# Performance work log

Hardware: AMD Instinct MI355X
Metric: run time of the kernel (lower is better)

Reference implementation:

```python
import jax, jax.numpy as jnp
import numpy as np
from jax.scipy.linalg import solve_triangular

H = 4          # num_heads
CHUNK = 64     # delta-rule chunk size (math-equivalent to any chunking)
NORM_EPS = 1e-5


def setup_inputs() -> dict:
    key = jax.random.key(0)
    ks = jax.random.split(key, 9)
    B, L, D = 4, 4096, 1024
    dk, dv = 512, 1024
    s = 0.02  # ~ xavier_uniform gain 2**-2.5 scale
    return {
        "hidden_states": jax.random.normal(ks[0], (B, L, D), jnp.float32),
        "conv_w": jax.random.normal(ks[1], (D, 4), jnp.float32) * 0.2,
        "Wq": jax.random.normal(ks[2], (D, dk), jnp.float32) * s,
        "Wk": jax.random.normal(ks[3], (D, dk), jnp.float32) * s,
        "Wv": jax.random.normal(ks[4], (D, dv), jnp.float32) * s,
        "Wb": jax.random.normal(ks[5], (D, H), jnp.float32) * s,
        "Wg": jax.random.normal(ks[6], (D, dv), jnp.float32) * s,
        "norm_w": jnp.ones((dv // H,), jnp.float32),
        "Wo": jax.random.normal(ks[7], (dv, D), jnp.float32) * s,
    }


def _l2norm(x):
    return x / jnp.clip(jnp.linalg.norm(x, axis=-1, keepdims=True), 1e-12)


def _deltanet_forward(hidden_states, conv_w, Wq, Wk, Wv, Wb, Wg, norm_w, Wo):
    B, L, D = hidden_states.shape
    Kc = conv_w.shape[1]
    dqh = Wq.shape[1] // H   # head qk dim (128)
    dvh = Wv.shape[1] // H   # head v dim (256)

    # shared causal depthwise short conv + silu (ShortConvolution)
    xp = jnp.pad(hidden_states, ((0, 0), (Kc - 1, 0), (0, 0)))
    h = sum(conv_w[:, i] * xp[:, i:i + L, :] for i in range(Kc))
    h = jax.nn.silu(h)

    q = (h @ Wq).reshape(B, L, H, dqh).transpose(0, 2, 1, 3)  # b h l d
    k = (h @ Wk).reshape(B, L, H, dqh).transpose(0, 2, 1, 3)
    v = (h @ Wv).reshape(B, L, H, dvh).transpose(0, 2, 1, 3)
    q = _l2norm(q)
    k = _l2norm(k)
    beta = jax.nn.sigmoid(h @ Wb).transpose(0, 2, 1)          # b h l

    qm = q.reshape(B * H, L, dqh)
    km = k.reshape(B * H, L, dqh)
    vm = v.reshape(B * H, L, dvh)
    bm = beta.reshape(B * H, L)

    Nc = L // CHUNK
    eye = jnp.eye(CHUNK, dtype=q.dtype)

    def per_head(qh, kh, vh, bh):
        qs = qh.reshape(Nc, CHUNK, dqh)
        ks_ = kh.reshape(Nc, CHUNK, dqh)
        vs = vh.reshape(Nc, CHUNK, dvh)
        bs = bh.reshape(Nc, CHUNK)

        def step(S, xs):
            qc, kc, vc, bc = xs
            kb = kc * bc[:, None]
            # (I + strict_tril(kb k^T)) U = beta*(V - K S)  -> exact delta rule
            A = jnp.tril(kb @ kc.T, -1)
            U = solve_triangular(eye + A, vc * bc[:, None] - kb @ S, lower=True)
            o = qc @ S + jnp.tril(qc @ kc.T) @ U
            return S + kc.T @ U, o

        S0 = jnp.zeros((dqh, dvh), qh.dtype)
        _, o = jax.lax.scan(step, S0, (qs, ks_, vs, bs))
        return o.reshape(L, dvh)

    o = jax.vmap(per_head)(qm, km, vm, bm)                    # (B*H, L, dvh)
    o = o.reshape(B, H, L, dvh).transpose(0, 2, 1, 3)         # b l h d

    # FusedRMSNormSwishGate: rmsnorm(o) * weight * silu(g)
    g = (h @ Wg).reshape(B, L, H, dvh)
    rms = o * jax.lax.rsqrt(jnp.mean(o * o, axis=-1, keepdims=True) + NORM_EPS)
    out = rms * norm_w * (g * jax.nn.sigmoid(g))
    return out.reshape(B, L, H * dvh) @ Wo


def reference(hidden_states, conv_w, Wq, Wk, Wv, Wb, Wg, norm_w, Wo):
    return _deltanet_forward(hidden_states, conv_w, Wq, Wk, Wv, Wb, Wg, norm_w, Wo)
```

## Files before the change

### kernel.cpp

```cpp
#include <hip/hip_runtime.h>
#include <math.h>

constexpr int Lseq = 4096, Dm = 1024, H = 4, DK = 512, DV = 1024;
constexpr int DQH = 128, DVH = 256, CH = 64, ROWS = 4 * 4096;
constexpr int QKS = 1024;

typedef unsigned short u16;
struct alignas(16) us8 { u16 u[8]; };
typedef __attribute__((ext_vector_type(8))) short bf16x8;
typedef __attribute__((ext_vector_type(4))) float f32x4;

__device__ __forceinline__ float sig_(float x) { return 1.f / (1.f + expf(-x)); }
__device__ __forceinline__ float b2f(u16 u) {
  union { float f; unsigned v; } x; x.v = (unsigned)u << 16; return x.f;
}
__device__ __forceinline__ u16 f2b(float f) {
  union { float f; unsigned v; } x; x.f = f;
  unsigned r = x.v + 0x7fffu + ((x.v >> 16) & 1u);
  return (u16)(r >> 16);
}
__device__ __forceinline__ void gld16(const u16* g, u16* l) {
  __builtin_amdgcn_global_load_lds(
      (const __attribute__((address_space(1))) void*)g,
      (__attribute__((address_space(3))) void*)l, 16, 0, 0);
}

__global__ void ws_sentinel_kernel(float* out, float v) { out[0] = v; }

__global__ __launch_bounds__(256) void prologue_kernel(
    const float* __restrict__ x, const float* __restrict__ w, u16* __restrict__ h,
    const float* __restrict__ Wq, const float* __restrict__ Wk,
    const float* __restrict__ Wv, const float* __restrict__ Wg,
    const float* __restrict__ Wo,
    u16* wq16, u16* wk16, u16* wv16, u16* wg16, u16* wo16) {
  __shared__ u16 T[32][66];
  const int t = threadIdx.x;
  if (blockIdx.x < 8192) {
    int idx = blockIdx.x * 256 + t;
    int d8 = (idx & 127) << 3;
    int row = idx >> 7;
    int l = row & (Lseq - 1), b = row >> 12;
    const float* xb = x + ((size_t)b << 22);
    float4 wv_[8];
#pragma unroll
    for (int j = 0; j < 2; ++j) {
      wv_[j * 4 + 0] = *(const float4*)&w[d8 * 4 + j * 16 + 0];
      wv_[j * 4 + 1] = *(const float4*)&w[d8 * 4 + j * 16 + 4];
      wv_[j * 4 + 2] = *(const float4*)&w[d8 * 4 + j * 16 + 8];
      wv_[j * 4 + 3] = *(const float4*)&w[d8 * 4 + j * 16 + 12];
    }
    float acc[8] = {0, 0, 0, 0, 0, 0, 0, 0};
#pragma unroll
    for (int i = 0; i < 4; ++i) {
      int li = l - 3 + i;
      if (li >= 0) {
        float4 x0 = *(const float4*)&xb[((size_t)li << 10) + d8];
        float4 x1 = *(const float4*)&xb[((size_t)li << 10) + d8 + 4];
        acc[0] = fmaf(((const float*)&wv_[0])[i], x0.x, acc[0]);
        acc[1] = fmaf(((const float*)&wv_[1])[i], x0.y, acc[1]);
        acc[2] = fmaf(((const float*)&wv_[2])[i], x0.z, acc[2]);
        acc[3] = fmaf(((const float*)&wv_[3])[i], x0.w, acc[3]);
        acc[4] = fmaf(((const float*)&wv_[4])[i], x1.x, acc[4]);
        acc[5] = fmaf(((const float*)&wv_[5])[i], x1.y, acc[5]);
        acc[6] = fmaf(((const float*)&wv_[6])[i], x1.z, acc[6]);
        acc[7] = fmaf(((const float*)&wv_[7])[i], x1.w, acc[7]);
      }
    }
    us8 o;
#pragma unroll
    for (int j = 0; j < 8; ++j) o.u[j] = f2b(acc[j] * sig_(acc[j]));
    *(us8*)&h[(size_t)row * Dm + d8] = o;
    return;
  }
  int bid = blockIdx.x - 8192;
  const float* in; u16* out; int N, K, b0;
  if (bid < 256)       { in = Wq; out = wq16; N = DK; K = Dm; b0 = bid; }
  else if (bid < 512)  { in = Wk; out = wk16; N = DK; K = Dm; b0 = bid - 256; }
  else if (bid < 1024) { in = Wv; out = wv16; N = DV; K = Dm; b0 = bid - 512; }
  else if (bid < 1536) { in = Wg; out = wg16; N = DV; K = Dm; b0 = bid - 1024; }
  else                 { in = Wo; out = wo16; N = Dm; K = DV; b0 = bid - 1536; }
  const int nbx = N / 64;
  const int k0 = (b0 / nbx) * 32, n0 = (b0 % nbx) * 64;
#pragma unroll
  for (int i = 0; i < 8; ++i) {
    int idx = t + i * 256;
    int kk = idx >> 6, nn = idx & 63;
    T[kk][nn] = f2b(in[(size_t)(k0 + kk) * N + n0 + nn]);
  }
  __syncthreads();
#pragma unroll
  for (int i = 0; i < 8; ++i) {
    int idx = t + i * 256;
    int kk = idx & 31, nn = idx >> 5;
    out[(size_t)(n0 + nn) * K + k0 + kk] = T[kk][nn];
  }
}

template <int MODE>
__device__ __forceinline__ void gemm_body(
    const u16* __restrict__ A, const u16* __restrict__ BT, void* __restrict__ Cv,
    int M, int N, int K, int bid, int nwg, u16* As, u16* Bs) {
  const int tid = threadIdx.x;
  const int wid = tid >> 6, lane = tid & 63;
  const int wr = wid >> 1, wc = wid & 1;
  const int fr = lane & 15, fk = lane >> 4;
  const int nbx = N >> 7;
  const int swz = (bid & 7) * (nwg >> 3) + (bid >> 3);
  const int row0 = (swz / nbx) * 128, col0 = (swz % nbx) * 128;

  int sr[4], sk[4];
#pragma unroll
  for (int i = 0; i < 4; ++i) {
    int s = i * 4 + wid;
    int r = s * 8 + (lane >> 3);
    sr[i] = r;
    sk[i] = ((lane & 7) ^ (r & 7)) << 3;
  }

  f32x4 acc[4][4];
#pragma unroll
  for (int i = 0; i < 4; ++i)
#pragma unroll
    for (int j = 0; j < 4; ++j) acc[i][j] = {0.f, 0.f, 0.f, 0.f};

  for (int k0 = 0; k0 < K; k0 += 64) {
#pragma unroll
    for (int i = 0; i < 4; ++i) {
      const int s = i * 4 + wid;
      gld16(&A[(size_t)(row0 + sr[i]) * K + k0 + sk[i]], &As[s * 512]);
      gld16(&BT[(size_t)(col0 + sr[i]) * K + k0 + sk[i]], &Bs[s * 512]);
    }
    __syncthreads();
#pragma unroll
    for (int kt = 0; kt < 2; ++kt) {
      bf16x8 af[4], bf[4];
#pragma unroll
      for (int mi = 0; mi < 4; ++mi) {
        int row = wr * 64 + mi * 16 + fr;
        af[mi] = *(const bf16x8*)&As[row * 64 + (((kt * 4 + fk) ^ (fr & 7)) << 3)];
      }
#pragma unroll
      for (int ni = 0; ni < 4; ++ni) {
        int row = wc * 64 + ni * 16 + fr;
        bf[ni] = *(const bf16x8*)&Bs[row * 64 + (((kt * 4 + fk) ^ (fr & 7)) << 3)];
      }
#pragma unroll
      for (int mi = 0; mi < 4; ++mi)
#pragma unroll
        for (int ni = 0; ni < 4; ++ni)
          acc[mi][ni] = __builtin_amdgcn_mfma_f32_16x16x32_bf16(
              af[mi], bf[ni], acc[mi][ni], 0, 0, 0);
    }
    __syncthreads();
  }

  if (MODE == 2) {
    __shared__ float ssh[2][128];
#pragma unroll
    for (int mi = 0; mi < 4; ++mi)
#pragma unroll
      for (int r = 0; r < 4; ++r) {
        float p = 0.f;
#pragma unroll
        for (int ni = 0; ni < 4; ++ni) p += acc[mi][ni][r] * acc[mi][ni][r];
        p += __shfl_xor(p, 1); p += __shfl_xor(p, 2);
        p += __shfl_xor(p, 4); p += __shfl_xor(p, 8);
        if (fr == 0) ssh[wc][wr * 64 + mi * 16 + fk * 4 + r] = p;
      }
    __syncthreads();
#pragma unroll
    for (int mi = 0; mi < 4; ++mi)
#pragma unroll
      for (int r = 0; r < 4; ++r) {
        int ridx = wr * 64 + mi * 16 + fk * 4 + r;
        float sc = 1.f / fmaxf(sqrtf(ssh[0][ridx] + ssh[1][ridx]), 1e-12f);
#pragma unroll
        for (int ni = 0; ni < 4; ++ni) acc[mi][ni][r] *= sc;
      }
  }

#pragma unroll
  for (int mi = 0; mi < 4; ++mi)
#pragma unroll
    for (int ni = 0; ni < 4; ++ni) {
      int col = col0 + wc * 64 + ni * 16 + fr;
#pragma unroll
      for (int r = 0; r < 4; ++r) {
        int row = row0 + wr * 64 + mi * 16 + fk * 4 + r;
        if (MODE == 1) ((float*)Cv)[(size_t)row * N + col] = acc[mi][ni][r];
        else           ((u16*)Cv)[(size_t)row * N + col] = f2b(acc[mi][ni][r]);
      }
    }
}

__global__ __launch_bounds__(256) void gemm_mfma_kernel(
    const u16* __restrict__ A, const u16* __restrict__ BT, void* __restrict__ Cv,
    int M, int N, int K) {
  __shared__ u16 As[128 * 64];
  __shared__ u16 Bs[128 * 64];
  gemm_body<1>(A, BT, Cv, M, N, K, blockIdx.x, gridDim.x, As, Bs);
}

__global__ __launch_bounds__(256) void proj_kernel(
    const u16* __restrict__ hb, const u16* __restrict__ wqk16,
    const u16* __restrict__ wv16, const float* __restrict__ Wb,
    u16* __restrict__ qk, u16* __restrict__ vb, float* __restrict__ beta) {
  __shared__ u16 As[128 * 64];
  __shared__ u16 Bs[128 * 64];
  const int bid = blockIdx.x;
  if (bid < 1024) {
    gemm_body<2>(hb, wqk16, qk, ROWS, QKS, Dm, bid, 1024, As, Bs);
    return;
  }
  if (bid < 2048) {
    gemm_body<0>(hb, wv16, vb, ROWS, DV, Dm, bid - 1024, 1024, As, Bs);
    return;
  }
  int row = (bid - 2048) * 4 + (threadIdx.x >> 6), lane = threadIdx.x & 63;
  const u16* hrow = hb + (size_t)row * Dm;
  float a0 = 0, a1 = 0, a2 = 0, a3 = 0;
  for (int k0 = 0; k0 < Dm; k0 += 64) {
    float hv = b2f(hrow[k0 + lane]);
    float4 wv = *(const float4*)&Wb[(size_t)(k0 + lane) * 4];
    a0 = fmaf(hv, wv.x, a0); a1 = fmaf(hv, wv.y, a1);
    a2 = fmaf(hv, wv.z, a2); a3 = fmaf(hv, wv.w, a3);
  }
#pragma unroll
  for (int off = 32; off; off >>= 1) {
    a0 += __shfl_down(a0, off); a1 += __shfl_down(a1, off);
    a2 += __shfl_down(a2, off); a3 += __shfl_down(a3, off);
  }
  if (lane == 0) {
    int b = row >> 12, l = row & (Lseq - 1);
    beta[((size_t)(b * H + 0)) * Lseq + l] = sig_(a0);
    beta[((size_t)(b * H + 1)) * Lseq + l] = sig_(a1);
    beta[((size_t)(b * H + 2)) * Lseq + l] = sig_(a2);
    beta[((size_t)(b * H + 3)) * Lseq + l] = sig_(a3);
  }
}

__global__ __launch_bounds__(256) void delta_prep_kernel(
    const u16* __restrict__ qk, u16* v, const float* __restrict__ beta,
    u16* __restrict__ Wout, u16* __restrict__ QKout) {
  __shared__ alignas(16) char lds0[18432];
  __shared__ alignas(16) char lds1[18432];
  __shared__ float Bc[64];
  float (*Am)[68] = (float(*)[68])lds0;
  float (*R)[68]  = (float(*)[68])lds1;
  u16 (*Th)[72]  = (u16(*)[72])lds0;
  u16 (*Tl)[72]  = (u16(*)[72])(lds0 + 9216);
  u16 (*XTh)[72] = (u16(*)[72])lds1;
  u16 (*XTl)[72] = (u16(*)[72])(lds1 + 9216);

  const int tid = threadIdx.x;
  const int wid = tid >> 6, lane = tid & 63;
  const int fr = lane & 15, fq = lane >> 4;
  const int bh = blockIdx.x >> 6, ch = blockIdx.x & 63;
  const int b = bh >> 2, hh = bh & 3;
  const int c0 = ch * CH;
  const u16* qbase = qk + (size_t)b * Lseq * QKS + hh * DQH;
  const u16* kbase = qk + (size_t)b * Lseq * QKS + 512 + hh * DQH;
  u16*       vbase = v + (size_t)b * Lseq * DV + hh * DVH;
  const float* bbase = beta + (size_t)bh * Lseq;
  u16* Wrow  = Wout  + ((size_t)bh * Lseq + c0) * DQH;
  u16* QKrow = QKout + ((size_t)bh * Lseq + c0) * CH;

  if (tid < 64) Bc[tid] = bbase[c0 + tid];
  for (int idx = tid; idx < 64 * 64; idx += 256) {
    int r = idx >> 6, c = idx & 63;
    R[r][c] = (r == c) ? 1.f : 0.f;
  }
  __syncthreads();

  {
    const int m0 = wid * 16;
    f32x4 accG[4], accQ[4];
#pragma unroll
    for (int ni = 0; ni < 4; ++ni) {
      accG[ni] = {0.f, 0.f, 0.f, 0.f};
      accQ[ni] = {0.f, 0.f, 0.f, 0.f};
    }
#pragma unroll
    for (int kt = 0; kt < 4; ++kt) {
      bf16x8 afk = *(const bf16x8*)&kbase[(size_t)(c0 + m0 + fr) * QKS + kt * 32 + fq * 8];
      bf16x8 afq = *(const bf16x8*)&qbase[(size_t)(c0 + m0 + fr) * QKS + kt * 32 + fq * 8];
#pragma unroll
      for (int ni = 0; ni < 4; ++ni) {
        bf16x8 bfk = *(const bf16x8*)&kbase[(size_t)(c0 + ni * 16 + fr) * QKS + kt * 32 + fq * 8];
        accG[ni] = __builtin_amdgcn_mfma_f32_16x16x32_bf16(afk, bfk, accG[ni], 0, 0, 0);
        accQ[ni] = __builtin_amdgcn_mfma_f32_16x16x32_bf16(afq, bfk, accQ[ni], 0, 0, 0);
      }
    }
#pragma unroll
    for (int ni = 0; ni < 4; ++ni)
#pragma unroll
      for (int i = 0; i < 4; ++i) {
        int row = m0 + fq * 4 + i, col = ni * 16 + fr;
        float br = Bc[row];
        Am[row][col] = (col < row) ? br * accG[ni][i] : 0.f;
        QKrow[(size_t)row * CH + col] = f2b((col <= row) ? accQ[ni][i] : 0.f);
      }
  }
  __syncthreads();

  for (int rb = 0; rb < 4; ++rb) {
    if (rb > 0) {
      const int c = tid & 63, g = tid >> 6;
      const int R0 = rb * 16, row = R0 + g * 4;
      float s0 = 0, s1 = 0, s2 = 0, s3 = 0;
      for (int m = 0; m < R0; ++m) {
        float uv = R[m][c];
        s0 = fmaf(Am[row + 0][m], uv, s0);
        s1 = fmaf(Am[row + 1][m], uv, s1);
        s2 = fmaf(Am[row + 2][m], uv, s2);
        s3 = fmaf(Am[row + 3][m], uv, s3);
      }
      R[row + 0][c] -= s0; R[row + 1][c] -= s1;
      R[row + 2][c] -= s2; R[row + 3][c] -= s3;
    }
    __syncthreads();
    if (tid < 64) {
      const int c = tid;
      for (int i = 1; i < 16; ++i) {
        const int row = rb * 16 + i;
        float s = R[row][c];
        for (int m = 0; m < i; ++m)
          s = fmaf(-Am[row][rb * 16 + m], R[rb * 16 + m][c], s);
        R[row][c] = s;
      }
    }
    __syncthreads();
  }

  for (int idx = tid; idx < 64 * 64; idx += 256) {
    int r = idx >> 6, c = idx & 63;
    float tv = R[r][c];
    u16 hh2 = f2b(tv);
    Th[r][c] = hh2;
    Tl[r][c] = f2b(tv - b2f(hh2));
  }
  __syncthreads();

  for (int p = 0; p < 6; ++p) {
    const int off = (p < 2) ? p * 64 : (p - 2) * 64;
    for (int idx = tid; idx < 64 * 64; idx += 256) {
      int d = idx & 63, m = idx >> 6;
      float xv;
      if (p < 2) xv = Bc[m] * b2f(kbase[(size_t)(c0 + m) * QKS + off + d]);
      else       xv = Bc[m] * b2f(vbase[(size_t)(c0 + m) * DV + off + d]);
      u16 hh2 = f2b(xv);
      XTh[d][m] = hh2;
      XTl[d][m] = f2b(xv - b2f(hh2));
    }
    __syncthreads();
    f32x4 acc[4];
#pragma unroll
    for (int tn = 0; tn < 4; ++tn) acc[tn] = {0.f, 0.f, 0.f, 0.f};
#pragma unroll
    for (int kt = 0; kt < 2; ++kt) {
      bf16x8 ah = *(const bf16x8*)&Th[wid * 16 + fr][kt * 32 + fq * 8];
      bf16x8 al = *(const bf16x8*)&Tl[wid * 16 + fr][kt * 32 + fq * 8];
#pragma unroll
      for (int tn = 0; tn < 4; ++tn) {
        bf16x8 xh = *(const bf16x8*)&XTh[tn * 16 + fr][kt * 32 + fq * 8];
        bf16x8 xl = *(const bf16x8*)&XTl[tn * 16 + fr][kt * 32 + fq * 8];
        acc[tn] = __builtin_amdgcn_mfma_f32_16x16x32_bf16(ah, xh, acc[tn], 0, 0, 0);
        acc[tn] = __builtin_amdgcn_mfma_f32_16x16x32_bf16(ah, xl, acc[tn], 0, 0, 0);
        acc[tn] = __builtin_amdgcn_mfma_f32_16x16x32_bf16(al, xh, acc[tn], 0, 0, 0);
      }
    }
#pragma unroll
    for (int tn = 0; tn < 4; ++tn)
#pragma unroll
      for (int i = 0; i < 4; ++i) {
        int row = wid * 16 + fq * 4 + i, col = tn * 16 + fr;
        if (p < 2) Wrow[(size_t)row * DQH + off + col] = f2b(-acc[tn][i]);
        else       vbase[(size_t)(c0 + row) * DV + off + col] = f2b(acc[tn][i]);
      }
    __syncthreads();
  }
}

__device__ __forceinline__ void scan_body(
    int sbid, const u16* __restrict__ qkp,
    const u16* __restrict__ Wb, const u16* __restrict__ QKb, u16* uo,
    u16 (*Kt)[72], u16 (*Sbt_hi)[136], u16 (*Sbt_lo)[136], u16 (*Ubt)[72]) {
  const int tid = threadIdx.x;
  const int wid = tid >> 6, lane = tid & 63;
  const int fr = lane & 15, fq = lane >> 4;
  const int m0w = 16 * (wid & 3);
  const int bh = sbid & 15, vblk = sbid >> 4;
  const int b = bh >> 2, hh = bh & 3;
  const u16* qbase = qkp + (size_t)b * Lseq * QKS + hh * DQH;
  const u16* kbase = qkp + (size_t)b * Lseq * QKS + 512 + hh * DQH;
  const u16* Wbase = Wb + (size_t)bh * Lseq * DQH;
  const u16* QKbase = QKb + (size_t)bh * Lseq * CH;
  u16* uobase = uo + (size_t)b * Lseq * DV + hh * DVH + vblk * 16;

  for (int i = tid; i < 16 * 136; i += 512) {
    (&Sbt_hi[0][0])[i] = 0; (&Sbt_lo[0][0])[i] = 0;
  }
  f32x4 Sfrag = {0.f, 0.f, 0.f, 0.f};

  const int kr0 = tid & 63, kd0 = (tid >> 6) << 3;
  const int kr1 = (tid + 512) & 63, kd1 = ((tid + 512) >> 6) << 3;

  us8 kpre0 = *(const us8*)&kbase[(size_t)kr0 * QKS + kd0];
  us8 kpre1 = *(const us8*)&kbase[(size_t)kr1 * QKS + kd1];
  bf16x8 fpre[4];
  bf16x8 qkpre0 = {}, qkpre1 = {};
  ushort4 u0pre = {};
  if (wid < 4) {
    const u16* wp = Wbase + (size_t)(m0w + fr) * DQH + fq * 8;
#pragma unroll
    for (int kt = 0; kt < 4; ++kt) fpre[kt] = *(const bf16x8*)&wp[kt * 32];
    const u16* up = uobase + (size_t)(m0w + fq * 4) * DV + fr;
    u0pre.x = up[0]; u0pre.y = up[(size_t)DV];
    u0pre.z = up[(size_t)2 * DV]; u0pre.w = up[(size_t)3 * DV];
  } else {
    const u16* qp = qbase + (size_t)(m0w + fr) * QKS + fq * 8;
#pragma unroll
    for (int kt = 0; kt < 4; ++kt) fpre[kt] = *(const bf16x8*)&qp[kt * 32];
    const u16* qkp2 = QKbase + (size_t)(m0w + fr) * CH + fq * 8;
    qkpre0 = *(const bf16x8*)&qkp2[0];
    qkpre1 = *(const bf16x8*)&qkp2[32];
  }
  __syncthreads();

  for (int c0 = 0; c0 < Lseq; c0 += CH) {
#pragma unroll
    for (int j = 0; j < 8; ++j) Kt[kd0 + j][kr0] = kpre0.u[j];
#pragma unroll
    for (int j = 0; j < 8; ++j) Kt[kd1 + j][kr1] = kpre1.u[j];

    bf16x8 fcur[4];
#pragma unroll
    for (int kt = 0; kt < 4; ++kt) fcur[kt] = fpre[kt];
    bf16x8 qkc0 = qkpre0, qkc1 = qkpre1;
    ushort4 u0c = u0pre;

    if (c0 + CH < Lseq) {
      const int cn = c0 + CH;
      kpre0 = *(const us8*)&kbase[(size_t)(cn + kr0) * QKS + kd0];
      kpre1 = *(const us8*)&kbase[(size_t)(cn + kr1) * QKS + kd1];
      if (wid < 4) {
        const u16* wp = Wbase + (size_t)(cn + m0w + fr) * DQH + fq * 8;
#pragma unroll
        for (int kt = 0; kt < 4; ++kt) fpre[kt] = *(const bf16x8*)&wp[kt * 32];
        const u16* up = uobase + (size_t)(cn + m0w + fq * 4) * DV + fr;
        u0pre.x = up[0]; u0pre.y = up[(size_t)DV];
        u0pre.z = up[(size_t)2 * DV]; u0pre.w = up[(size_t)3 * DV];
      } else {
        const u16* qp = qbase + (size_t)(cn + m0w + fr) * QKS + fq * 8;
#pragma unroll
        for (int kt = 0; kt < 4; ++kt) fpre[kt] = *(const bf16x8*)&qp[kt * 32];
        const u16* qkp2 = QKbase + (size_t)(cn + m0w + fr) * CH + fq * 8;
        qkpre0 = *(const bf16x8*)&qkp2[0];
        qkpre1 = *(const bf16x8*)&qkp2[32];
      }
    }

    f32x4 acc, accB;
    if (wid < 4) {
      acc[0] = b2f(u0c.x); acc[1] = b2f(u0c.y);
      acc[2] = b2f(u0c.z); acc[3] = b2f(u0c.w);
      accB = (f32x4){0.f, 0.f, 0.f, 0.f};
      __builtin_amdgcn_s_setprio(1);
#pragma unroll
      for (int kt = 0; kt < 2; ++kt) {
        bf16x8 sh = *(const bf16x8*)&Sbt_hi[fr][kt * 32 + fq * 8];
        bf16x8 sl = *(const bf16x8*)&Sbt_lo[fr][kt * 32 + fq * 8];
        acc = __builtin_amdgcn_mfma_f32_16x16x32_bf16(fcur[kt], sh, acc, 0, 0, 0);
        acc = __builtin_amdgcn_mfma_f32_16x16x32_bf16(fcur[kt], sl, acc, 0, 0, 0);
      }
#pragma unroll
      for (int kt = 2; kt < 4; ++kt) {
        bf16x8 sh = *(const bf16x8*)&Sbt_hi[fr][kt * 32 + fq * 8];
        bf16x8 sl = *(const bf16x8*)&Sbt_lo[fr][kt * 32 + fq * 8];
        accB = __builtin_amdgcn_mfma_f32_16x16x32_bf16(fcur[kt], sh, accB, 0, 0, 0);
        accB = __builtin_amdgcn_mfma_f32_16x16x32_bf16(fcur[kt], sl, accB, 0, 0, 0);
      }
      __builtin_amdgcn_s_setprio(0);
      ushort4 ub = {f2b(acc[0] + accB[0]), f2b(acc[1] + accB[1]),
                    f2b(acc[2] + accB[2]), f2b(acc[3] + accB[3])};
      *(ushort4*)&Ubt[fr][m0w + fq * 4] = ub;
    } else {
      acc = (f32x4){0.f, 0.f, 0.f, 0.f};
      accB = (f32x4){0.f, 0.f, 0.f, 0.f};
#pragma unroll
      for (int kt = 0; kt < 2; ++kt) {
        bf16x8 sh = *(const bf16x8*)&Sbt_hi[fr][kt * 32 + fq * 8];
        acc = __builtin_amdgcn_mfma_f32_16x16x32_bf16(fcur[kt], sh, acc, 0, 0, 0);
      }
#pragma unroll
      for (int kt = 2; kt < 4; ++kt) {
        bf16x8 sh = *(const bf16x8*)&Sbt_hi[fr][kt * 32 + fq * 8];
        accB = __builtin_amdgcn_mfma_f32_16x16x32_bf16(fcur[kt], sh, accB, 0, 0, 0);
      }
    }
    __syncthreads();

    if (wid >= 4) {
      bf16x8 uf0 = *(const bf16x8*)&Ubt[fr][fq * 8];
      bf16x8 uf1 = *(const bf16x8*)&Ubt[fr][32 + fq * 8];
      acc  = __builtin_amdgcn_mfma_f32_16x16x32_bf16(qkc0, uf0, acc, 0, 0, 0);
      accB = __builtin_amdgcn_mfma_f32_16x16x32_bf16(qkc1, uf1, accB, 0, 0, 0);
      u16* op = uobase + (size_t)(c0 + m0w + fq * 4) * DV + fr;
      op[0] = f2b(acc[0] + accB[0]);
      op[(size_t)DV] = f2b(acc[1] + accB[1]);
      op[(size_t)2 * DV] = f2b(acc[2] + accB[2]);
      op[(size_t)3 * DV] = f2b(acc[3] + accB[3]);
    }
    __builtin_amdgcn_s_setprio(1);
#pragma unroll
    for (int kt = 0; kt < 2; ++kt) {
      bf16x8 kf = *(const bf16x8*)&Kt[16 * wid + fr][kt * 32 + fq * 8];
      bf16x8 uf = *(const bf16x8*)&Ubt[fr][kt * 32 + fq * 8];
      Sfrag = __builtin_amdgcn_mfma_f32_16x16x32_bf16(kf, uf, Sfrag, 0, 0, 0);
    }
    __builtin_amdgcn_s_setprio(0);
    ushort4 shv, slv;
#pragma unroll
    for (int i = 0; i < 4; ++i) {
      float s = Sfrag[i];
      u16 hpart = f2b(s);
      ((u16*)&shv)[i] = hpart;
      ((u16*)&slv)[i] = f2b(s - b2f(hpart));
    }
    *(ushort4*)&Sbt_hi[fr][16 * wid + fq * 4] = shv;
    *(ushort4*)&Sbt_lo[fr][16 * wid + fq * 4] = slv;
    __syncthreads();
  }
}

__global__ __launch_bounds__(512) void delta_scan_kernel(
    const u16* __restrict__ qk, const u16* __restrict__ Wb,
    const u16* __restrict__ QKb, u16* uo) {
  __shared__ alignas(16) u16 Kt[128][72];
  __shared__ alignas(16) u16 Sbt_hi[16][136];
  __shared__ alignas(16) u16 Sbt_lo[16][136];
  __shared__ alignas(16) u16 Ubt[16][72];
  scan_body(blockIdx.x, qk, Wb, QKb, uo, Kt, Sbt_hi, Sbt_lo, Ubt);
}

__global__ __launch_bounds__(512) void scan_wg_kernel(
    const u16* __restrict__ qk, const u16* __restrict__ Wb,
    const u16* __restrict__ QKb, u16* uo,
    const u16* __restrict__ A, const u16* __restrict__ BT, u16* __restrict__ C) {
  __shared__ alignas(16) u16 Kt[128][72];
  __shared__ alignas(16) u16 Sbt_hi[16][136];
  __shared__ alignas(16) u16 Sbt_lo[16][136];
  __shared__ alignas(16) u16 Ubt[16][72];
  __shared__ u16 As[128 * 64];
  __shared__ u16 Bs[128 * 64];

  if (blockIdx.x < 256) {
    scan_body(blockIdx.x, qk, Wb, QKb, uo, Kt, Sbt_hi, Sbt_lo, Ubt);
    return;
  }
  const int tid = threadIdx.x;
  const int wid = tid >> 6, lane = tid & 63;
  const int wr = wid >> 2, wc = wid & 3;
  const int fr = lane & 15, fk = lane >> 4;
  const int nbx = DV >> 7;
  const int gbid = blockIdx.x - 256, nwg = 1024;
  const int swz = (gbid & 7) * (nwg >> 3) + (gbid >> 3);
  const int row0 = (swz / nbx) * 128, col0 = (swz % nbx) * 128;

  int sr[2], sk[2];
#pragma unroll
  for (int i = 0; i < 2; ++i) {
    int s = i * 8 + wid;
    int r = s * 8 + (lane >> 3);
    sr[i] = r;
    sk[i] = ((lane & 7) ^ (r & 7)) << 3;
  }

  f32x4 acc[4][2];
#pragma unroll
  for (int i = 0; i < 4; ++i)
#pragma unroll
    for (int j = 0; j < 2; ++j) acc[i][j] = {0.f, 0.f, 0.f, 0.f};

  for (int k0 = 0; k0 < Dm; k0 += 64) {
#pragma unroll
    for (int i = 0; i < 2; ++i) {
      const int s = i * 8 + wid;
      gld16(&A[(size_t)(row0 + sr[i]) * Dm + k0 + sk[i]], &As[s * 512]);
      gld16(&BT[(size_t)(col0 + sr[i]) * Dm + k0 + sk[i]], &Bs[s * 512]);
    }
    __syncthreads();
#pragma unroll
    for (int kt = 0; kt < 2; ++kt) {
      bf16x8 af[4], bf[2];
#pragma unroll
      for (int mi = 0; mi < 4; ++mi) {
        int row = wr * 64 + mi * 16 + fr;
        af[mi] = *(const bf16x8*)&As[row * 64 + (((kt * 4 + fk) ^ (fr & 7)) << 3)];
      }
#pragma unroll
      for (int ni = 0; ni < 2; ++ni) {
        int row = wc * 32 + ni * 16 + fr;
        bf[ni] = *(const bf16x8*)&Bs[row * 64 + (((kt * 4 + fk) ^ (fr & 7)) << 3)];
      }
#pragma unroll
      for (int mi = 0; mi < 4; ++mi)
#pragma unroll
        for (int ni = 0; ni < 2; ++ni)
          acc[mi][ni] = __builtin_amdgcn_mfma_f32_16x16x32_bf16(
              af[mi], bf[ni], acc[mi][ni], 0, 0, 0);
    }
    __syncthreads();
  }
#pragma unroll
  for (int mi = 0; mi < 4; ++mi)
#pragma unroll
    for (int ni = 0; ni < 2; ++ni) {
      int col = col0 + wc * 32 + ni * 16 + fr;
#pragma unroll
      for (int r = 0; r < 4; ++r) {
        int row = row0 + wr * 64 + mi * 16 + fk * 4 + r;
        C[(size_t)row * DV + col] = f2b(acc[mi][ni][r]);
      }
    }
}

__global__ __launch_bounds__(256) void gate_kernel(
    const u16* og, const u16* __restrict__ g,
    const float* __restrict__ nw, u16* out) {
  int idx = blockIdx.x * 4 + (threadIdx.x >> 6), lane = threadIdx.x & 63;
  size_t base = (size_t)(idx >> 2) * DV + (size_t)(idx & 3) * DVH + (size_t)lane * 4;
  ushort4 o4 = *(const ushort4*)&og[base];
  float ox = b2f(o4.x), oy = b2f(o4.y), oz = b2f(o4.z), ow = b2f(o4.w);
  float ss = ox * ox + oy * oy + oz * oz + ow * ow;
#pragma unroll
  for (int off = 32; off; off >>= 1) ss += __shfl_xor(ss, off);
  float r = 1.f / sqrtf(ss * (1.f / DVH) + 1e-5f);
  ushort4 g4 = *(const ushort4*)&g[base];
  float gx = b2f(g4.x), gy = b2f(g4.y), gz = b2f(g4.z), gw = b2f(g4.w);
  float4 wv = *(const float4*)&nw[lane * 4];
  ushort4 res;
  res.x = f2b(ox * r * wv.x * (gx * sig_(gx)));
  res.y = f2b(oy * r * wv.y * (gy * sig_(gy)));
  res.z = f2b(oz * r * wv.z * (gz * sig_(gz)));
  res.w = f2b(ow * r * wv.w * (gw * sig_(gw)));
  *(ushort4*)&out[base] = res;
}

__global__ __launch_bounds__(256) void gemm_bf16_kernel(
    const u16* __restrict__ A, const u16* __restrict__ BT, void* __restrict__ Cv,
    int M, int N, int K) {
  __shared__ u16 As[128 * 64];
  __shared__ u16 Bs[128 * 64];
  gemm_body<0>(A, BT, Cv, M, N, K, blockIdx.x, gridDim.x, As, Bs);
}

extern "C" void kernel_launch(void* const* d_in, const int* in_sizes, int n_in,
                              void* d_out, int out_size, void* d_ws, size_t ws_size,
                              hipStream_t stream) {
  (void)in_sizes; (void)n_in; (void)out_size;
  const float* x  = (const float*)d_in[0];
  const float* cw = (const float*)d_in[1];
  const float* Wq = (const float*)d_in[2];
  const float* Wk = (const float*)d_in[3];
  const float* Wv = (const float*)d_in[4];
  const float* Wb = (const float*)d_in[5];
  const float* Wg = (const float*)d_in[6];
  const float* nw = (const float*)d_in[7];
  const float* Wo = (const float*)d_in[8];
  float* out = (float*)d_out;

  u16* hb  = (u16*)d_ws;
  u16* qkb = hb + (size_t)ROWS * Dm;
  u16* vb  = qkb + (size_t)ROWS * QKS;
  float* bbuf = (float*)(vb + (size_t)ROWS * DV);
  u16* Wbuf  = (u16*)(bbuf + (size_t)ROWS * H);
  u16* QKbuf = Wbuf + (size_t)16 * Lseq * DQH;
  u16* wq16 = QKbuf + (size_t)16 * Lseq * CH;
  u16* wk16 = wq16 + (size_t)Dm * DK;
  u16* wv16 = wk16 + (size_t)Dm * DK;
  u16* wg16 = wv16 + (size_t)Dm * DV;
  u16* wo16 = wg16 + (size_t)Dm * DV;
  u16* gb2  = wo16 + (size_t)DV * Dm;
  u16* gb   = qkb;

  const size_t need = (size_t)ROWS * (Dm + QKS + DV) * 2 + (size_t)ROWS * H * 4
                    + (size_t)16 * Lseq * (DQH + CH) * 2
                    + ((size_t)Dm * (DK * 2 + DV * 3)) * 2;
  const size_t need2 = need + (size_t)ROWS * DV * 2;
  if (ws_size < need) {
    ws_sentinel_kernel<<<1, 1, 0, stream>>>(out, (float)ws_size);
    return;
  }
  const bool fused = (ws_size >= need2);

  prologue_kernel<<<10240, 256, 0, stream>>>(x, cw, hb, Wq, Wk, Wv, Wg, Wo,
                                             wq16, wk16, wv16, wg16, wo16);
  proj_kernel<<<6144, 256, 0, stream>>>(hb, wq16, wv16, Wb, qkb, vb, bbuf);

  delta_prep_kernel<<<1024, 256, 0, stream>>>(qkb, vb, bbuf, Wbuf, QKbuf);

  if (fused) {
    scan_wg_kernel<<<1280, 512, 0, stream>>>(qkb, Wbuf, QKbuf, vb, hb, wg16, gb2);
    gate_kernel<<<ROWS * H / 4, 256, 0, stream>>>(vb, gb2, nw, vb);
  } else {
    delta_scan_kernel<<<256, 512, 0, stream>>>(qkb, Wbuf, QKbuf, vb);
    gemm_bf16_kernel<<<(DV / 128) * (ROWS / 128), 256, 0, stream>>>(hb, wg16, gb, ROWS, DV, Dm);
    gate_kernel<<<ROWS * H / 4, 256, 0, stream>>>(vb, gb, nw, vb);
  }

  gemm_mfma_kernel<<<(Dm / 128) * (ROWS / 128), 256, 0, stream>>>(vb, wo16, out, ROWS, Dm, DV);
}
```

Before: 467.1 us.

## Precompute per-chunk state transition matrices to shorten the sequential delta scan

```diff
diff --git a/kernel.cpp b/kernel.cpp
--- a/kernel.cpp
+++ b/kernel.cpp
@@ -381,6 +381,323 @@
   }
 }
 
+__global__ __launch_bounds__(256) void mk_kernel(
+    const u16* __restrict__ qk, u16* Wn, const u16* __restrict__ QKb,
+    u16* __restrict__ Mb) {
+  __shared__ alignas(16) u16 Kt[128][72];
+  __shared__ alignas(16) u16 WT[128][72];
+  const int tid = threadIdx.x;
+  const int wid = tid >> 6, lane = tid & 63;
+  const int fr = lane & 15, fq = lane >> 4;
+  const int bh = blockIdx.x >> 6, ch = blockIdx.x & 63;
+  const int b = bh >> 2, hh = bh & 3;
+  const int c0 = ch * CH;
+  const u16* qbase = qk + (size_t)b * Lseq * QKS + hh * DQH;
+  const u16* kbase = qk + (size_t)b * Lseq * QKS + 512 + hh * DQH;
+  u16* Wrow = Wn + ((size_t)bh * Lseq + c0) * DQH;
+  const u16* QKrow = QKb + ((size_t)bh * Lseq + c0) * CH;
+  u16* Mrow = Mb + (size_t)(bh * 64 + ch) * (128 * 128);
+
+#pragma unroll
+  for (int i = 0; i < 4; ++i) {
+    int id = tid + i * 256;
+    int r = id & 63, d8 = (id >> 6) << 3;
+    us8 kv = *(const us8*)&kbase[(size_t)(c0 + r) * QKS + d8];
+#pragma unroll
+    for (int j = 0; j < 8; ++j) Kt[d8 + j][r] = kv.u[j];
+  }
+#pragma unroll
+  for (int i = 0; i < 4; ++i) {
+    int id = tid + i * 256;
+    int r = id >> 4, n8 = (id & 15) << 3;
+    us8 wv = *(const us8*)&Wrow[(size_t)r * DQH + n8];
+#pragma unroll
+    for (int j = 0; j < 8; ++j) WT[n8 + j][r] = wv.u[j];
+  }
+  __syncthreads();
+
+#pragma unroll
+  for (int mt = 0; mt < 2; ++mt) {
+    const int mrow = 32 * wid + 16 * mt;
+    bf16x8 a0 = *(const bf16x8*)&Kt[mrow + fr][fq * 8];
+    bf16x8 a1 = *(const bf16x8*)&Kt[mrow + fr][32 + fq * 8];
+    f32x4 acc[8];
+#pragma unroll
+    for (int nt = 0; nt < 8; ++nt) acc[nt] = {0.f, 0.f, 0.f, 0.f};
+#pragma unroll
+    for (int nt = 0; nt < 8; ++nt) {
+      bf16x8 b0 = *(const bf16x8*)&WT[nt * 16 + fr][fq * 8];
+      bf16x8 b1 = *(const bf16x8*)&WT[nt * 16 + fr][32 + fq * 8];
+      acc[nt] = __builtin_amdgcn_mfma_f32_16x16x32_bf16(a0, b0, acc[nt], 0, 0, 0);
+      acc[nt] = __builtin_amdgcn_mfma_f32_16x16x32_bf16(a1, b1, acc[nt], 0, 0, 0);
+    }
+#pragma unroll
+    for (int nt = 0; nt < 8; ++nt)
+#pragma unroll
+      for (int i = 0; i < 4; ++i)
+        Mrow[(size_t)(mrow + fq * 4 + i) * 128 + nt * 16 + fr] = f2b(acc[nt][i]);
+  }
+
+  {
+    const int m0 = 16 * wid;
+    bf16x8 a0 = *(const bf16x8*)&QKrow[(size_t)(m0 + fr) * CH + fq * 8];
+    bf16x8 a1 = *(const bf16x8*)&QKrow[(size_t)(m0 + fr) * CH + 32 + fq * 8];
+    f32x4 acc[8];
+#pragma unroll
+    for (int nt = 0; nt < 8; ++nt) acc[nt] = {0.f, 0.f, 0.f, 0.f};
+#pragma unroll
+    for (int nt = 0; nt < 8; ++nt) {
+      bf16x8 b0 = *(const bf16x8*)&WT[nt * 16 + fr][fq * 8];
+      bf16x8 b1 = *(const bf16x8*)&WT[nt * 16 + fr][32 + fq * 8];
+      acc[nt] = __builtin_amdgcn_mfma_f32_16x16x32_bf16(a0, b0, acc[nt], 0, 0, 0);
+      acc[nt] = __builtin_amdgcn_mfma_f32_16x16x32_bf16(a1, b1, acc[nt], 0, 0, 0);
+    }
+    __syncthreads();
+#pragma unroll
+    for (int nt = 0; nt < 8; ++nt)
+#pragma unroll
+      for (int i = 0; i < 4; ++i) {
+        int row = m0 + fq * 4 + i, col = nt * 16 + fr;
+        float qv = b2f(qbase[(size_t)(c0 + row) * QKS + col]);
+        Wrow[(size_t)row * DQH + col] = f2b(qv + acc[nt][i]);
+      }
+  }
+}
+
+__device__ __forceinline__ void scan2_body(
+    int sbid, const u16* __restrict__ qk, const u16* __restrict__ Qp,
+    const u16* __restrict__ QKb, const u16* __restrict__ Mb, u16* uo,
+    u16 (*Kt)[72], u16 (*Sbt_hi)[136], u16 (*Sbt_lo)[136], u16 (*U0t)[72]) {
+  const int tid = threadIdx.x;
+  const int wid = tid >> 6, lane = tid & 63;
+  const int fr = lane & 15, fq = lane >> 4;
+  const int m0w = 16 * (wid & 3);
+  const int bh = sbid & 15, vblk = sbid >> 4;
+  const int b = bh >> 2, hh = bh & 3;
+  const u16* kbase = qk + (size_t)b * Lseq * QKS + 512 + hh * DQH;
+  const u16* Qpbase = Qp + (size_t)bh * Lseq * DQH;
+  const u16* QKbase = QKb + (size_t)bh * Lseq * CH;
+  const u16* Mbase = Mb + (size_t)bh * 64 * (128 * 128);
+  u16* uobase = uo + (size_t)b * Lseq * DV + hh * DVH + vblk * 16;
+
+  for (int i = tid; i < 16 * 136; i += 512) {
+    (&Sbt_hi[0][0])[i] = 0; (&Sbt_lo[0][0])[i] = 0;
+  }
+  f32x4 Sfrag = {0.f, 0.f, 0.f, 0.f};
+
+  const int kr0 = tid & 63, kd0 = (tid >> 6) << 3;
+  const int kr1 = (tid + 512) & 63, kd1 = ((tid + 512) >> 6) << 3;
+  const int ur = tid & 63, uc = tid >> 6;
+
+  us8 kpre0 = *(const us8*)&kbase[(size_t)kr0 * QKS + kd0];
+  us8 kpre1 = *(const us8*)&kbase[(size_t)kr1 * QKS + kd1];
+  u16 upre0 = uobase[(size_t)ur * DV + uc];
+  u16 upre1 = uobase[(size_t)ur * DV + uc + 8];
+  bf16x8 mpre[4];
+#pragma unroll
+  for (int kt = 0; kt < 4; ++kt)
+    mpre[kt] = *(const bf16x8*)&Mbase[(size_t)(16 * wid + fr) * 128 + kt * 32 + fq * 8];
+  bf16x8 qppre[4];
+  bf16x8 qkpre0 = {}, qkpre1 = {};
+  if (wid >= 4) {
+    const u16* qp = Qpbase + (size_t)(m0w + fr) * DQH + fq * 8;
+#pragma unroll
+    for (int kt = 0; kt < 4; ++kt) qppre[kt] = *(const bf16x8*)&qp[kt * 32];
+    const u16* qkp = QKbase + (size_t)(m0w + fr) * CH + fq * 8;
+    qkpre0 = *(const bf16x8*)&qkp[0];
+    qkpre1 = *(const bf16x8*)&qkp[32];
+  }
+#pragma unroll
+  for (int j = 0; j < 8; ++j) Kt[kd0 + j][kr0] = kpre0.u[j];
+#pragma unroll
+  for (int j = 0; j < 8; ++j) Kt[kd1 + j][kr1] = kpre1.u[j];
+  U0t[uc][ur] = upre0;
+  U0t[uc + 8][ur] = upre1;
+  __syncthreads();
+
+  for (int ch = 0; ch < 64; ++ch) {
+    const int c0 = ch * CH;
+    bf16x8 mcur[4];
+#pragma unroll
+    for (int kt = 0; kt < 4; ++kt) mcur[kt] = mpre[kt];
+    bf16x8 qpc[4];
+    bf16x8 qkc0 = qkpre0, qkc1 = qkpre1;
+    if (wid >= 4) {
+#pragma unroll
+      for (int kt = 0; kt < 4; ++kt) qpc[kt] = qppre[kt];
+    }
+    if (ch + 1 < 64) {
+      const int cn = c0 + CH;
+      kpre0 = *(const us8*)&kbase[(size_t)(cn + kr0) * QKS + kd0];
+      kpre1 = *(const us8*)&kbase[(size_t)(cn + kr1) * QKS + kd1];
+      upre0 = uobase[(size_t)(cn + ur) * DV + uc];
+      upre1 = uobase[(size_t)(cn + ur) * DV + uc + 8];
+#pragma unroll
+      for (int kt = 0; kt < 4; ++kt)
+        mpre[kt] = *(const bf16x8*)&Mbase[(size_t)(ch + 1) * (128 * 128) +
+                                          (size_t)(16 * wid + fr) * 128 + kt * 32 + fq * 8];
+      if (wid >= 4) {
+        const u16* qp = Qpbase + (size_t)(cn + m0w + fr) * DQH + fq * 8;
+#pragma unroll
+        for (int kt = 0; kt < 4; ++kt) qppre[kt] = *(const bf16x8*)&qp[kt * 32];
+        const u16* qkp = QKbase + (size_t)(cn + m0w + fr) * CH + fq * 8;
+        qkpre0 = *(const bf16x8*)&qkp[0];
+        qkpre1 = *(const bf16x8*)&qkp[32];
+      }
+    }
+    f32x4 zacc = {0.f, 0.f, 0.f, 0.f};
+    __builtin_amdgcn_s_setprio(1);
+#pragma unroll
+    for (int kt = 0; kt < 2; ++kt) {
+      bf16x8 kf = *(const bf16x8*)&Kt[16 * wid + fr][kt * 32 + fq * 8];
+      bf16x8 uf = *(const bf16x8*)&U0t[fr][kt * 32 + fq * 8];
+      zacc = __builtin_amdgcn_mfma_f32_16x16x32_bf16(kf, uf, zacc, 0, 0, 0);
+    }
+    f32x4 accA = Sfrag, accB = {0.f, 0.f, 0.f, 0.f};
+#pragma unroll
+    for (int kt = 0; kt < 2; ++kt) {
+      bf16x8 sh = *(const bf16x8*)&Sbt_hi[fr][kt * 32 + fq * 8];
+      bf16x8 sl = *(const bf16x8*)&Sbt_lo[fr][kt * 32 + fq * 8];
+      accA = __builtin_amdgcn_mfma_f32_16x16x32_bf16(mcur[kt], sh, accA, 0, 0, 0);
+      accA = __builtin_amdgcn_mfma_f32_16x16x32_bf16(mcur[kt], sl, accA, 0, 0, 0);
+    }
+#pragma unroll
+    for (int kt = 2; kt < 4; ++kt) {
+      bf16x8 sh = *(const bf16x8*)&Sbt_hi[fr][kt * 32 + fq * 8];
+      bf16x8 sl = *(const bf16x8*)&Sbt_lo[fr][kt * 32 + fq * 8];
+      accB = __builtin_amdgcn_mfma_f32_16x16x32_bf16(mcur[kt], sh, accB, 0, 0, 0);
+      accB = __builtin_amdgcn_mfma_f32_16x16x32_bf16(mcur[kt], sl, accB, 0, 0, 0);
+    }
+    __builtin_amdgcn_s_setprio(0);
+    f32x4 oacc = {0.f, 0.f, 0.f, 0.f};
+    if (wid >= 4) {
+#pragma unroll
+      for (int kt = 0; kt < 4; ++kt) {
+        bf16x8 sh = *(const bf16x8*)&Sbt_hi[fr][kt * 32 + fq * 8];
+        oacc = __builtin_amdgcn_mfma_f32_16x16x32_bf16(qpc[kt], sh, oacc, 0, 0, 0);
+      }
+      bf16x8 uf0 = *(const bf16x8*)&U0t[fr][fq * 8];
+      bf16x8 uf1 = *(const bf16x8*)&U0t[fr][32 + fq * 8];
+      oacc = __builtin_amdgcn_mfma_f32_16x16x32_bf16(qkc0, uf0, oacc, 0, 0, 0);
+      oacc = __builtin_amdgcn_mfma_f32_16x16x32_bf16(qkc1, uf1, oacc, 0, 0, 0);
+    }
+    __syncthreads();
+
+    Sfrag[0] = accA[0] + accB[0] + zacc[0];
+    Sfrag[1] = accA[1] + accB[1] + zacc[1];
+    Sfrag[2] = accA[2] + accB[2] + zacc[2];
+    Sfrag[3] = accA[3] + accB[3] + zacc[3];
+    ushort4 shv, slv;
+#pragma unroll
+    for (int i = 0; i < 4; ++i) {
+      float s = Sfrag[i];
+      u16 hpart = f2b(s);
+      ((u16*)&shv)[i] = hpart;
+      ((u16*)&slv)[i] = f2b(s - b2f(hpart));
+    }
+    *(ushort4*)&Sbt_hi[fr][16 * wid + fq * 4] = shv;
+    *(ushort4*)&Sbt_lo[fr][16 * wid + fq * 4] = slv;
+    if (wid >= 4) {
+      u16* op = uobase + (size_t)(c0 + m0w + fq * 4) * DV + fr;
+      op[0] = f2b(oacc[0]);
+      op[(size_t)DV] = f2b(oacc[1]);
+      op[(size_t)2 * DV] = f2b(oacc[2]);
+      op[(size_t)3 * DV] = f2b(oacc[3]);
+    }
+    if (ch + 1 < 64) {
+#pragma unroll
+      for (int j = 0; j < 8; ++j) Kt[kd0 + j][kr0] = kpre0.u[j];
+#pragma unroll
+      for (int j = 0; j < 8; ++j) Kt[kd1 + j][kr1] = kpre1.u[j];
+      U0t[uc][ur] = upre0;
+      U0t[uc + 8][ur] = upre1;
+    }
+    __syncthreads();
+  }
+}
+
+__global__ __launch_bounds__(512) void scan2_wg_kernel(
+    const u16* __restrict__ qk, const u16* __restrict__ Qp,
+    const u16* __restrict__ QKb, const u16* __restrict__ Mb, u16* uo,
+    const u16* __restrict__ A, const u16* __restrict__ BT, u16* __restrict__ C) {
+  __shared__ alignas(16) u16 Kt[128][72];
+  __shared__ alignas(16) u16 Sbt_hi[16][136];
+  __shared__ alignas(16) u16 Sbt_lo[16][136];
+  __shared__ alignas(16) u16 U0t[16][72];
+  __shared__ u16 As[128 * 64];
+  __shared__ u16 Bs[128 * 64];
+
+  if (blockIdx.x < 256) {
+    scan2_body(blockIdx.x, qk, Qp, QKb, Mb, uo, Kt, Sbt_hi, Sbt_lo, U0t);
+    return;
+  }
+  const int tid = threadIdx.x;
+  const int wid = tid >> 6, lane = tid & 63;
+  const int wr = wid >> 2, wc = wid & 3;
+  const int fr = lane & 15, fk = lane >> 4;
+  const int nbx = DV >> 7;
+  const int gbid = blockIdx.x - 256, nwg = 1024;
+  const int swz = (gbid & 7) * (nwg >> 3) + (gbid >> 3);
+  const int row0 = (swz / nbx) * 128, col0 = (swz % nbx) * 128;
+
+  int sr[2], sk[2];
+#pragma unroll
+  for (int i = 0; i < 2; ++i) {
+    int s = i * 8 + wid;
+    int r = s * 8 + (lane >> 3);
+    sr[i] = r;
+    sk[i] = ((lane & 7) ^ (r & 7)) << 3;
+  }
+
+  f32x4 acc[4][2];
+#pragma unroll
+  for (int i = 0; i < 4; ++i)
+#pragma unroll
+    for (int j = 0; j < 2; ++j) acc[i][j] = {0.f, 0.f, 0.f, 0.f};
+
+  for (int k0 = 0; k0 < Dm; k0 += 64) {
+#pragma unroll
+    for (int i = 0; i < 2; ++i) {
+      const int s = i * 8 + wid;
+      gld16(&A[(size_t)(row0 + sr[i]) * Dm + k0 + sk[i]], &As[s * 512]);
+      gld16(&BT[(size_t)(col0 + sr[i]) * Dm + k0 + sk[i]], &Bs[s * 512]);
+    }
+    __syncthreads();
+#pragma unroll
+    for (int kt = 0; kt < 2; ++kt) {
+      bf16x8 af[4], bf[2];
+#pragma unroll
+      for (int mi = 0; mi < 4; ++mi) {
+        int row = wr * 64 + mi * 16 + fr;
+        af[mi] = *(const bf16x8*)&As[row * 64 + (((kt * 4 + fk) ^ (fr & 7)) << 3)];
+      }
+#pragma unroll
+      for (int ni = 0; ni < 2; ++ni) {
+        int row = wc * 32 + ni * 16 + fr;
+        bf[ni] = *(const bf16x8*)&Bs[row * 64 + (((kt * 4 + fk) ^ (fr & 7)) << 3)];
+      }
+#pragma unroll
+      for (int mi = 0; mi < 4; ++mi)
+#pragma unroll
+        for (int ni = 0; ni < 2; ++ni)
+          acc[mi][ni] = __builtin_amdgcn_mfma_f32_16x16x32_bf16(
+              af[mi], bf[ni], acc[mi][ni], 0, 0, 0);
+    }
+    __syncthreads();
+  }
+#pragma unroll
+  for (int mi = 0; mi < 4; ++mi)
+#pragma unroll
+    for (int ni = 0; ni < 2; ++ni) {
+      int col = col0 + wc * 32 + ni * 16 + fr;
+#pragma unroll
+      for (int r = 0; r < 4; ++r) {
+        int row = row0 + wr * 64 + mi * 16 + fk * 4 + r;
+        C[(size_t)row * DV + col] = f2b(acc[mi][ni][r]);
+      }
+    }
+}
+
 __device__ __forceinline__ void scan_body(
     int sbid, const u16* __restrict__ qkp,
     const u16* __restrict__ Wb, const u16* __restrict__ QKb, u16* uo,
@@ -682,25 +999,30 @@
   u16* wg16 = wv16 + (size_t)Dm * DV;
   u16* wo16 = wg16 + (size_t)Dm * DV;
   u16* gb2  = wo16 + (size_t)DV * Dm;
+  u16* Mbuf = gb2 + (size_t)ROWS * DV;
   u16* gb   = qkb;
 
   const size_t need = (size_t)ROWS * (Dm + QKS + DV) * 2 + (size_t)ROWS * H * 4
                     + (size_t)16 * Lseq * (DQH + CH) * 2
                     + ((size_t)Dm * (DK * 2 + DV * 3)) * 2;
   const size_t need2 = need + (size_t)ROWS * DV * 2;
+  const size_t need3 = need2 + (size_t)16 * 64 * 128 * 128 * 2;
   if (ws_size < need) {
     ws_sentinel_kernel<<<1, 1, 0, stream>>>(out, (float)ws_size);
     return;
   }
-  const bool fused = (ws_size >= need2);
 
   prologue_kernel<<<10240, 256, 0, stream>>>(x, cw, hb, Wq, Wk, Wv, Wg, Wo,
                                              wq16, wk16, wv16, wg16, wo16);
   proj_kernel<<<6144, 256, 0, stream>>>(hb, wq16, wv16, Wb, qkb, vb, bbuf);
-
   delta_prep_kernel<<<1024, 256, 0, stream>>>(qkb, vb, bbuf, Wbuf, QKbuf);
 
-  if (fused) {
+  if (ws_size >= need3) {
+    mk_kernel<<<1024, 256, 0, stream>>>(qkb, Wbuf, QKbuf, Mbuf);
+    scan2_wg_kernel<<<1280, 512, 0, stream>>>(qkb, Wbuf, QKbuf, Mbuf, vb,
+                                              hb, wg16, gb2);
+    gate_kernel<<<ROWS * H / 4, 256, 0, stream>>>(vb, gb2, nw, vb);
+  } else if (ws_size >= need2) {
     scan_wg_kernel<<<1280, 512, 0, stream>>>(qkb, Wbuf, QKbuf, vb, hb, wg16, gb2);
     gate_kernel<<<ROWS * H / 4, 256, 0, stream>>>(vb, gb2, nw, vb);
   } else {
```

Result: slower. 582.0 us (+24.6%).
